# Performance work log

Measured on AMD Instinct MI355X. Metric: run time of the kernel, lower is better.

## Reference

```python
import jax, jax.numpy as jnp
import numpy as np

TOK, IN, OUT = 4096, 4096, 12288


def setup_inputs() -> dict:
    key = jax.random.key(0)
    k1, k2, k3, k4 = jax.random.split(key, 4)
    x = jax.random.normal(k1, (TOK, IN), dtype=jnp.float32)
    # int8 weight stored [out, in] (module transposes to this layout)
    weight = jax.random.randint(k2, (OUT, IN), -128, 128, dtype=jnp.int32).astype(jnp.int8)
    # per-output-channel dequant scale (positive, realistic magnitude)
    weight_scale = jax.random.uniform(k3, (OUT,), dtype=jnp.float32) * 0.02 + 1e-3
    bias = jax.random.normal(k4, (OUT,), dtype=jnp.float32) * 0.01
    return {"x": x, "weight": weight, "weight_scale": weight_scale, "bias": bias}


def reference(x, weight, weight_scale, bias):
    # --- dynamic per-token activation quantization ---
    amax = jnp.max(jnp.abs(x), axis=-1, keepdims=True)          # [TOK, 1]
    act_scale = jnp.maximum(amax / 127.0, 1e-8)                  # per-token scale
    x_q = jnp.clip(jnp.round(x / act_scale), -128, 127).astype(jnp.int8)
    # --- int8 GEMM accumulating in int32: y = x_q @ W^T ---
    acc = jax.lax.dot_general(
        x_q, weight,
        dimension_numbers=(((1,), (1,)), ((), ())),
        preferred_element_type=jnp.int32,
    )                                                            # [TOK, OUT] int32
    # --- dequant: per-token act scale * per-channel weight scale, + bias ---
    return acc.astype(jnp.float32) * act_scale * weight_scale + bias
```

## Files before the change

kernel.cpp:

```cpp
#include <hip/hip_runtime.h>
#include <stdint.h>

#define TOK  4096
#define KIN  4096
#define NOUT 12288

#define BM  256
#define BN  256
#define BKB 128
#define NKT (KIN / BKB)

typedef __attribute__((ext_vector_type(4))) int int32x4;

__global__ __launch_bounds__(256) void repack_w(const int* __restrict__ w32,
                                                int8_t* __restrict__ w8)
{
    const size_t i = (size_t)blockIdx.x * 256 + threadIdx.x;
    const int4 v = ((const int4*)w32)[i];
    unsigned pack = ((unsigned)(uint8_t)(int8_t)v.x)
                  | ((unsigned)(uint8_t)(int8_t)v.y << 8)
                  | ((unsigned)(uint8_t)(int8_t)v.z << 16)
                  | ((unsigned)(uint8_t)(int8_t)v.w << 24);
    ((int*)w8)[i] = (int)pack;
}

__global__ __launch_bounds__(256) void quant_rows(const float* __restrict__ x,
                                                  int8_t* __restrict__ xq,
                                                  float* __restrict__ ascale)
{
    const int row = blockIdx.x;
    const int tid = threadIdx.x;
    const float4* xr = (const float4*)(x + (size_t)row * KIN);

    float4 v[4];
    float m = 0.0f;
#pragma unroll
    for (int i = 0; i < 4; ++i) {
        v[i] = xr[tid + 256 * i];
        m = fmaxf(m, fmaxf(fmaxf(fabsf(v[i].x), fabsf(v[i].y)),
                           fmaxf(fabsf(v[i].z), fabsf(v[i].w))));
    }
#pragma unroll
    for (int off = 32; off > 0; off >>= 1)
        m = fmaxf(m, __shfl_down(m, off, 64));
    __shared__ float wm[4];
    if ((tid & 63) == 0) wm[tid >> 6] = m;
    __syncthreads();
    const float amax = fmaxf(fmaxf(wm[0], wm[1]), fmaxf(wm[2], wm[3]));
    const float s   = fmaxf(amax / 127.0f, 1e-8f);
    const float inv = 1.0f / s;
    if (tid == 0) ascale[row] = s;

    int* out32 = (int*)(xq + (size_t)row * KIN);
#pragma unroll
    for (int i = 0; i < 4; ++i) {
        float c[4] = {v[i].x, v[i].y, v[i].z, v[i].w};
        unsigned pack = 0;
#pragma unroll
        for (int j = 0; j < 4; ++j) {
            float r = rintf(c[j] * inv);
            r = fminf(fmaxf(r, -128.0f), 127.0f);
            pack |= ((unsigned)(uint8_t)(int8_t)(int)r) << (8 * j);
        }
        out32[tid + 256 * i] = (int)pack;
    }
}

#define GLOAD_LDS16(g, l)                                                     \
    __builtin_amdgcn_global_load_lds(                                         \
        (const __attribute__((address_space(1))) unsigned int*)(g),           \
        (__attribute__((address_space(3))) unsigned int*)(l), 16, 0, 0)

#define STAGE_A(bufb, R0, kk)                                                 \
    GLOAD_LDS16(gA + (size_t)(R0) * KIN + (kk),                               \
                lA + (bufb) * 32768 + (R0) * 128)
#define STAGE_B(bufb, s, R0, kk)                                              \
    GLOAD_LDS16(gB + (size_t)(R0) * KIN + (kk) + (s) * 64,                    \
                lB + (bufb) * 32768 + (s) * 16384 + (R0) * 64)

#define PHASE(cur, mh, ks, STAGES, TAILWAIT)                                  \
    {                                                                         \
        const int abase = (cur) * 32768 + (mh) * 8192 + ((ks) ? aA1 : aA0);   \
        const int bbase = (cur) * 32768 + (ks) * 16384 + bA;                  \
        int32x4 af[4], bf[4];                                                 \
        _Pragma("unroll")                                                     \
        for (int u = 0; u < 4; ++u)                                           \
            af[u] = *(const int32x4*)(As + abase + u * 2048);                 \
        _Pragma("unroll")                                                     \
        for (int u = 0; u < 4; ++u)                                           \
            bf[u] = *(const int32x4*)(Bs + bbase + u * 1024);                 \
        STAGES;                                                               \
        __builtin_amdgcn_s_barrier();                                         \
        asm volatile("s_waitcnt lgkmcnt(0)" ::: "memory");                    \
        __builtin_amdgcn_sched_barrier(0);                                    \
        __builtin_amdgcn_s_setprio(1);                                        \
        _Pragma("unroll")                                                     \
        for (int fi = 0; fi < 4; ++fi)                                        \
            _Pragma("unroll")                                                 \
            for (int fj = 0; fj < 4; ++fj)                                    \
                acc[(mh) * 4 + fi][fj] =                                      \
                    __builtin_amdgcn_mfma_i32_16x16x64_i8(                    \
                        af[fi], bf[fj], acc[(mh) * 4 + fi][fj], 0, 0, 0);     \
        __builtin_amdgcn_s_setprio(0);                                        \
        TAILWAIT;                                                             \
        __builtin_amdgcn_s_barrier();                                         \
        asm volatile("" ::: "memory");                                        \
    }

__global__ __launch_bounds__(512, 2) void gemm_i8(const int8_t* __restrict__ A,
                                                  const int8_t* __restrict__ B,
                                                  const float* __restrict__ ascale,
                                                  const float* __restrict__ wscale,
                                                  const float* __restrict__ bias,
                                                  float* __restrict__ C)
{
    __shared__ __align__(16) int8_t As[2 * BM * BKB];
    __shared__ __align__(16) int8_t Bs[2 * 2 * BN * 64];

    const int tid  = (int)threadIdx.x;
    const int lane = tid & 63;
    const int wave = tid >> 6;
    const int quad = lane >> 4;
    const int l16  = lane & 15;
    const int wr   = wave >> 2;
    const int wc   = wave & 3;

    const int nbx  = NOUT / BN;
    const int wgid = (int)blockIdx.x;
    const int swz  = (wgid & 7) * (((TOK / BM) * nbx) >> 3) + (wgid >> 3);
    const int bx   = swz % nbx;
    const int by   = swz / nbx;
    const int m0   = by * BM;
    const int n0   = bx * BN;

    int32x4 acc[8][4];
#pragma unroll
    for (int i = 0; i < 8; ++i)
#pragma unroll
        for (int j = 0; j < 4; ++j) acc[i][j] = (int32x4){0, 0, 0, 0};

    const int arow = tid >> 3;
    const int8_t* gA = A + (size_t)(m0 + arow) * KIN
                         + (((tid & 7) ^ (arow & 7)) << 4);
    const int brow = tid >> 2;
    const int8_t* gB = B + (size_t)(n0 + brow) * KIN
                         + ((((tid & 3) ^ ((tid >> 3) & 3))) << 4);
    int8_t* lA = As + tid * 16;
    int8_t* lB = Bs + tid * 16;

    const int aA0 = (wr * 128 + l16) * 128 + (((0 + quad) ^ (l16 & 7)) << 4);
    const int aA1 = (wr * 128 + l16) * 128 + (((4 + quad) ^ (l16 & 7)) << 4);
    const int bA  = (wc * 64 + l16) * 64 + ((quad ^ ((l16 >> 1) & 3)) << 4);

    STAGE_A(0, 0, 0);      STAGE_A(0, 128, 0);
    STAGE_A(0, 64, 0);     STAGE_A(0, 192, 0);
    STAGE_B(0, 0, 0, 0);   STAGE_B(0, 0, 128, 0);
    STAGE_B(0, 1, 0, 0);   STAGE_B(0, 1, 128, 0);
    STAGE_B(1, 0, 0, BKB); STAGE_B(1, 0, 128, BKB);
    STAGE_A(1, 64, BKB);   STAGE_A(1, 192, BKB);
    asm volatile("s_waitcnt vmcnt(4)" ::: "memory");
    __builtin_amdgcn_s_barrier();
    asm volatile("" ::: "memory");

#pragma unroll 1
    for (int g = 0; g < NKT; g += 2) {
        const int k1 = (g + 1) * BKB;
        const int k2 = (g + 2 < NKT ? g + 2 : NKT - 1) * BKB;
        const int k3 = (g + 3 < NKT ? g + 3 : NKT - 1) * BKB;
        PHASE(0, 0, 0, { STAGE_A(1, 0, k1);    STAGE_A(1, 128, k1);
                         STAGE_B(1, 1, 0, k1); STAGE_B(1, 1, 128, k1); }, )
        PHASE(0, 1, 0, , )
        PHASE(0, 1, 1, { STAGE_B(0, 0, 0, k2); STAGE_B(0, 0, 128, k2); }, )
        PHASE(0, 0, 1, { STAGE_A(0, 64, k2);   STAGE_A(0, 192, k2); },
              asm volatile("s_waitcnt vmcnt(4)" ::: "memory"))
        PHASE(1, 0, 0, { STAGE_A(0, 0, k2);    STAGE_A(0, 128, k2);
                         STAGE_B(0, 1, 0, k2); STAGE_B(0, 1, 128, k2); }, )
        PHASE(1, 1, 0, , )
        PHASE(1, 1, 1, { STAGE_B(1, 0, 0, k3); STAGE_B(1, 0, 128, k3); }, )
        PHASE(1, 0, 1, { STAGE_A(1, 64, k3);   STAGE_A(1, 192, k3); },
              asm volatile("s_waitcnt vmcnt(4)" ::: "memory"))
    }

#pragma unroll
    for (int fi = 0; fi < 8; ++fi) {
        const int mb = m0 + wr * 128 + fi * 16 + quad * 4;
        const float as0 = ascale[mb + 0];
        const float as1 = ascale[mb + 1];
        const float as2 = ascale[mb + 2];
        const float as3 = ascale[mb + 3];
#pragma unroll
        for (int fj = 0; fj < 4; ++fj) {
            const int n = n0 + wc * 64 + fj * 16 + l16;
            const float wsn = wscale[n];
            const float bn  = bias[n];
            float* Cp = C + (size_t)mb * NOUT + n;
            Cp[0 * (size_t)NOUT] = (float)acc[fi][fj][0] * as0 * wsn + bn;
            Cp[1 * (size_t)NOUT] = (float)acc[fi][fj][1] * as1 * wsn + bn;
            Cp[2 * (size_t)NOUT] = (float)acc[fi][fj][2] * as2 * wsn + bn;
            Cp[3 * (size_t)NOUT] = (float)acc[fi][fj][3] * as3 * wsn + bn;
        }
    }
}

extern "C" void kernel_launch(void* const* d_in, const int* in_sizes, int n_in,
                              void* d_out, int out_size, void* d_ws, size_t ws_size,
                              hipStream_t stream)
{
    (void)in_sizes; (void)n_in; (void)out_size; (void)ws_size;
    const float* x      = (const float*)d_in[0];
    const int*   w32    = (const int*)d_in[1];
    const float* wscale = (const float*)d_in[2];
    const float* bias   = (const float*)d_in[3];
    float*       out    = (float*)d_out;

    int8_t* xq     = (int8_t*)d_ws;
    float*  ascale = (float*)((char*)d_ws + (size_t)TOK * KIN);
    int8_t* w8     = (int8_t*)((char*)d_ws + (size_t)TOK * KIN + 65536);

    repack_w<<<(size_t)NOUT * KIN / 4 / 256, 256, 0, stream>>>(w32, w8);
    quant_rows<<<TOK, 256, 0, stream>>>(x, xq, ascale);
    gemm_i8<<<(TOK / BM) * (NOUT / BN), 512, 0, stream>>>(xq, w8, ascale,
                                                          wscale, bias, out);
}
```

Baseline: 570.9 us.

## Switch int8 GEMM to 32x32x32 MFMA with reworked LDS fragment loads

Replaces the 16x16x64 int8 MFMA tiling with 32x32x32 int8 MFMAs. Each wave now holds 4x2 32x32 accumulator tiles and needs fewer LDS fragment reads per FLOP. B fragments are reused across two phases, and the explicit lgkmcnt(0) wait and sched_barrier are dropped so the compiler can schedule LDS loads itself. Global staging is also rebalanced across phases, and the epilogue is rewritten for the 32x32 output layout. The main risk is that weaker manual scheduling control lets the compiler insert waits badly.

```diff
diff --git a/kernel.cpp b/kernel.cpp
--- a/kernel.cpp
+++ b/kernel.cpp
@@ -10,7 +10,8 @@
 #define BKB 128
 #define NKT (KIN / BKB)
 
-typedef __attribute__((ext_vector_type(4))) int int32x4;
+typedef __attribute__((ext_vector_type(4)))  int int32x4;
+typedef __attribute__((ext_vector_type(16))) int int32x16;
 
 __global__ __launch_bounds__(256) void repack_w(const int* __restrict__ w32,
                                                 int8_t* __restrict__ w8)
@@ -78,31 +79,43 @@
     GLOAD_LDS16(gB + (size_t)(R0) * KIN + (kk) + (s) * 64,                    \
                 lB + (bufb) * 32768 + (s) * 16384 + (R0) * 64)
 
-#define PHASE(cur, mh, ks, STAGES, TAILWAIT)                                  \
+#define LOAD_AF(cur, mh, ks)                                                  \
+    af[0] = *(const int32x4*)(aP[(ks)*2+0] + (cur)*32768 + ((mh)*64+ 0)*128); \
+    af[1] = *(const int32x4*)(aP[(ks)*2+0] + (cur)*32768 + ((mh)*64+32)*128); \
+    af[2] = *(const int32x4*)(aP[(ks)*2+1] + (cur)*32768 + ((mh)*64+ 0)*128); \
+    af[3] = *(const int32x4*)(aP[(ks)*2+1] + (cur)*32768 + ((mh)*64+32)*128);
+
+#define LOAD_BF(cur, ks)                                                      \
+    bf[0] = *(const int32x4*)(bP[0] + (cur)*32768 + (ks)*16384 +    0);       \
+    bf[1] = *(const int32x4*)(bP[0] + (cur)*32768 + (ks)*16384 + 2048);       \
+    bf[2] = *(const int32x4*)(bP[1] + (cur)*32768 + (ks)*16384 +    0);       \
+    bf[3] = *(const int32x4*)(bP[1] + (cur)*32768 + (ks)*16384 + 2048);
+
+#define MFMA32(a, b, c) __builtin_amdgcn_mfma_i32_32x32x32_i8((a), (b), (c), 0, 0, 0)
+
+#define DO_MFMA(mh)                                                           \
+    acc[(mh)*2+0][0] = MFMA32(af[0], bf[0], acc[(mh)*2+0][0]);                \
+    acc[(mh)*2+0][1] = MFMA32(af[0], bf[1], acc[(mh)*2+0][1]);                \
+    acc[(mh)*2+1][0] = MFMA32(af[1], bf[0], acc[(mh)*2+1][0]);                \
+    acc[(mh)*2+1][1] = MFMA32(af[1], bf[1], acc[(mh)*2+1][1]);                \
+    acc[(mh)*2+0][0] = MFMA32(af[2], bf[2], acc[(mh)*2+0][0]);                \
+    acc[(mh)*2+0][1] = MFMA32(af[2], bf[3], acc[(mh)*2+0][1]);                \
+    acc[(mh)*2+1][0] = MFMA32(af[3], bf[2], acc[(mh)*2+1][0]);                \
+    acc[(mh)*2+1][1] = MFMA32(af[3], bf[3], acc[(mh)*2+1][1]);
+
+#define PHASE(cur, mh, ks, LOADBF, STAGES, TAILWAIT)                          \
     {                                                                         \
-        const int abase = (cur) * 32768 + (mh) * 8192 + ((ks) ? aA1 : aA0);   \
-        const int bbase = (cur) * 32768 + (ks) * 16384 + bA;                  \
-        int32x4 af[4], bf[4];                                                 \
-        _Pragma("unroll")                                                     \
-        for (int u = 0; u < 4; ++u)                                           \
-            af[u] = *(const int32x4*)(As + abase + u * 2048);                 \
-        _Pragma("unroll")                                                     \
-        for (int u = 0; u < 4; ++u)                                           \
-            bf[u] = *(const int32x4*)(Bs + bbase + u * 1024);                 \
+        LOADBF;                                                               \
+        LOAD_AF(cur, mh, ks);                                                 \
         STAGES;                                                               \
+        asm volatile("" ::: "memory");                                        \
         __builtin_amdgcn_s_barrier();                                         \
-        asm volatile("s_waitcnt lgkmcnt(0)" ::: "memory");                    \
-        __builtin_amdgcn_sched_barrier(0);                                    \
+        asm volatile("" ::: "memory");                                        \
         __builtin_amdgcn_s_setprio(1);                                        \
-        _Pragma("unroll")                                                     \
-        for (int fi = 0; fi < 4; ++fi)                                        \
-            _Pragma("unroll")                                                 \
-            for (int fj = 0; fj < 4; ++fj)                                    \
-                acc[(mh) * 4 + fi][fj] =                                      \
-                    __builtin_amdgcn_mfma_i32_16x16x64_i8(                    \
-                        af[fi], bf[fj], acc[(mh) * 4 + fi][fj], 0, 0, 0);     \
+        DO_MFMA(mh);                                                          \
         __builtin_amdgcn_s_setprio(0);                                        \
         TAILWAIT;                                                             \
+        asm volatile("" ::: "memory");                                        \
         __builtin_amdgcn_s_barrier();                                         \
         asm volatile("" ::: "memory");                                        \
     }
@@ -120,8 +133,8 @@
     const int tid  = (int)threadIdx.x;
     const int lane = tid & 63;
     const int wave = tid >> 6;
-    const int quad = lane >> 4;
-    const int l16  = lane & 15;
+    const int hi   = lane >> 5;
+    const int l5   = lane & 31;
     const int wr   = wave >> 2;
     const int wc   = wave & 3;
 
@@ -133,11 +146,10 @@
     const int m0   = by * BM;
     const int n0   = bx * BN;
 
-    int32x4 acc[8][4];
-#pragma unroll
-    for (int i = 0; i < 8; ++i)
-#pragma unroll
-        for (int j = 0; j < 4; ++j) acc[i][j] = (int32x4){0, 0, 0, 0};
+    const int32x16 zero = {0,0,0,0,0,0,0,0,0,0,0,0,0,0,0,0};
+    int32x16 acc[4][2];
+#pragma unroll
+    for (int i = 0; i < 4; ++i) { acc[i][0] = zero; acc[i][1] = zero; }
 
     const int arow = tid >> 3;
     const int8_t* gA = A + (size_t)(m0 + arow) * KIN
@@ -148,9 +160,16 @@
     int8_t* lA = As + tid * 16;
     int8_t* lB = Bs + tid * 16;
 
-    const int aA0 = (wr * 128 + l16) * 128 + (((0 + quad) ^ (l16 & 7)) << 4);
-    const int aA1 = (wr * 128 + l16) * 128 + (((4 + quad) ^ (l16 & 7)) << 4);
-    const int bA  = (wc * 64 + l16) * 64 + ((quad ^ ((l16 >> 1) & 3)) << 4);
+    const int8_t* aP[4];
+#pragma unroll
+    for (int i = 0; i < 4; ++i)
+        aP[i] = As + (wr * 128 + l5) * 128 + (((i * 2 + hi) ^ (l5 & 7)) << 4);
+    const int8_t* bP[2];
+#pragma unroll
+    for (int i = 0; i < 2; ++i)
+        bP[i] = Bs + (wc * 64 + l5) * 64 + (((i * 2 + hi) ^ ((l5 >> 1) & 3)) << 4);
+
+    int32x4 af[4], bf[4];
 
     STAGE_A(0, 0, 0);      STAGE_A(0, 128, 0);
     STAGE_A(0, 64, 0);     STAGE_A(0, 192, 0);
@@ -167,37 +186,47 @@
         const int k1 = (g + 1) * BKB;
         const int k2 = (g + 2 < NKT ? g + 2 : NKT - 1) * BKB;
         const int k3 = (g + 3 < NKT ? g + 3 : NKT - 1) * BKB;
-        PHASE(0, 0, 0, { STAGE_A(1, 0, k1);    STAGE_A(1, 128, k1);
-                         STAGE_B(1, 1, 0, k1); STAGE_B(1, 1, 128, k1); }, )
-        PHASE(0, 1, 0, , )
-        PHASE(0, 1, 1, { STAGE_B(0, 0, 0, k2); STAGE_B(0, 0, 128, k2); }, )
-        PHASE(0, 0, 1, { STAGE_A(0, 64, k2);   STAGE_A(0, 192, k2); },
+        PHASE(0, 0, 0, LOAD_BF(0, 0),
+              { STAGE_A(1, 0, k1);    STAGE_A(1, 128, k1); }, )
+        PHASE(0, 1, 0, ,
+              { STAGE_B(1, 1, 0, k1); STAGE_B(1, 1, 128, k1); }, )
+        PHASE(0, 1, 1, LOAD_BF(0, 1),
+              { STAGE_B(0, 0, 0, k2); STAGE_B(0, 0, 128, k2); }, )
+        PHASE(0, 0, 1, ,
+              { STAGE_A(0, 64, k2);   STAGE_A(0, 192, k2); },
               asm volatile("s_waitcnt vmcnt(4)" ::: "memory"))
-        PHASE(1, 0, 0, { STAGE_A(0, 0, k2);    STAGE_A(0, 128, k2);
-                         STAGE_B(0, 1, 0, k2); STAGE_B(0, 1, 128, k2); }, )
-        PHASE(1, 1, 0, , )
-        PHASE(1, 1, 1, { STAGE_B(1, 0, 0, k3); STAGE_B(1, 0, 128, k3); }, )
-        PHASE(1, 0, 1, { STAGE_A(1, 64, k3);   STAGE_A(1, 192, k3); },
+        PHASE(1, 0, 0, LOAD_BF(1, 0),
+              { STAGE_A(0, 0, k2);    STAGE_A(0, 128, k2); }, )
+        PHASE(1, 1, 0, ,
+              { STAGE_B(0, 1, 0, k2); STAGE_B(0, 1, 128, k2); }, )
+        PHASE(1, 1, 1, LOAD_BF(1, 1),
+              { STAGE_B(1, 0, 0, k3); STAGE_B(1, 0, 128, k3); }, )
+        PHASE(1, 0, 1, ,
+              { STAGE_A(1, 64, k3);   STAGE_A(1, 192, k3); },
               asm volatile("s_waitcnt vmcnt(4)" ::: "memory"))
     }
 
-#pragma unroll
-    for (int fi = 0; fi < 8; ++fi) {
-        const int mb = m0 + wr * 128 + fi * 16 + quad * 4;
-        const float as0 = ascale[mb + 0];
-        const float as1 = ascale[mb + 1];
-        const float as2 = ascale[mb + 2];
-        const float as3 = ascale[mb + 3];
-#pragma unroll
-        for (int fj = 0; fj < 4; ++fj) {
-            const int n = n0 + wc * 64 + fj * 16 + l16;
-            const float wsn = wscale[n];
-            const float bn  = bias[n];
-            float* Cp = C + (size_t)mb * NOUT + n;
-            Cp[0 * (size_t)NOUT] = (float)acc[fi][fj][0] * as0 * wsn + bn;
-            Cp[1 * (size_t)NOUT] = (float)acc[fi][fj][1] * as1 * wsn + bn;
-            Cp[2 * (size_t)NOUT] = (float)acc[fi][fj][2] * as2 * wsn + bn;
-            Cp[3 * (size_t)NOUT] = (float)acc[fi][fj][3] * as3 * wsn + bn;
+    const int nn0 = n0 + wc * 64 + l5;
+    const float wsn0 = wscale[nn0],      bn0 = bias[nn0];
+    const float wsn1 = wscale[nn0 + 32], bn1 = bias[nn0 + 32];
+#pragma unroll
+    for (int R = 0; R < 4; ++R) {
+#pragma unroll
+        for (int rq = 0; rq < 4; ++rq) {
+            const int mb = m0 + wr * 128 + R * 32 + rq * 8 + hi * 4;
+            const float a0 = ascale[mb + 0];
+            const float a1 = ascale[mb + 1];
+            const float a2 = ascale[mb + 2];
+            const float a3 = ascale[mb + 3];
+            float* Cp = C + (size_t)mb * NOUT + nn0;
+            Cp[0 * (size_t)NOUT]      = (float)acc[R][0][rq*4+0] * a0 * wsn0 + bn0;
+            Cp[1 * (size_t)NOUT]      = (float)acc[R][0][rq*4+1] * a1 * wsn0 + bn0;
+            Cp[2 * (size_t)NOUT]      = (float)acc[R][0][rq*4+2] * a2 * wsn0 + bn0;
+            Cp[3 * (size_t)NOUT]      = (float)acc[R][0][rq*4+3] * a3 * wsn0 + bn0;
+            Cp[0 * (size_t)NOUT + 32] = (float)acc[R][1][rq*4+0] * a0 * wsn1 + bn1;
+            Cp[1 * (size_t)NOUT + 32] = (float)acc[R][1][rq*4+1] * a1 * wsn1 + bn1;
+            Cp[2 * (size_t)NOUT + 32] = (float)acc[R][1][rq*4+2] * a2 * wsn1 + bn1;
+            Cp[3 * (size_t)NOUT + 32] = (float)acc[R][1][rq*4+3] * a3 * wsn1 + bn1;
         }
     }
 }
```

Result: no change. 566.6 us (-0.8%).
